# Kernel optimization log

Hardware: AMD Instinct MI355X
Metric: run time of the kernel (lower is better)

The kernel has to match this reference:

```python
import jax, jax.numpy as jnp
import numpy as np

N_STEPS = 100
E_PERT = 0.001
K_GATE = 500.0

# (a1,a2,a3,a4, b1,b2,b3,b4, xi_E, xi_I) per oscillator type
_COEFFS = {
    1: (0.0, 5.0, 5.0, 1.0, 0.0, -1.0, 1.0, 0.0, 0.0, 0.0),
    2: (0.5, 0.55, 0.55, -0.5, 0.5, -0.55, -0.55, -0.5, 0.0, 0.0),
    3: (-5.0, 5.0, 5.0, -5.0, 1.0, -1.0, -1.0, 1.0, 0.0, 0.0),
    4: (1.0, 1.0, 1.0, -1.0, -1.0, -1.0, -1.0, 1.0, 0.0, 0.0),
    5: (5.0, -5.0, -5.0, 5.0, -1.0, 1.0, 1.0, -1.0, 0.0, 0.0),
    6: (-1.0, -1.0, -1.0, 1.0, 1.0, 1.0, 1.0, -1.0, 0.0, 0.0),
    7: (1.0, -1.0, -1.0, 1.0, -1.0, 1.0, 1.0, -1.0, 0.0, 0.0),
    8: (-1.0, 1.0, 1.0, -1.0, 1.0, -1.0, -1.0, 1.0, 0.0, 0.0),
}

def _tanh5(x):
    return jnp.tanh(5.0 * x)

def lee_oscillator(x, oscillator_type):
    a1, a2, a3, a4, b1, b2, b3, b4, xi_E, xi_I = _COEFFS[int(oscillator_type)]
    shape = x.shape
    xf = x.reshape(-1)
    sim = xf + E_PERT * jnp.sign(xf)
    gate = jnp.exp(-K_GATE * sim * sim)   # exp(-k*sim^2), constant over steps
    omega = _tanh5(sim)                   # Omega[t+1] = tanh(5*sim), constant

    E0 = jnp.full_like(xf, 0.2)
    I0 = jnp.zeros_like(xf)
    L0 = jnp.full_like(xf, 0.2)

    def step(carry, _):
        E, I, L = carry
        E1 = _tanh5(a1 * L + a2 * E - a3 * I + a4 * sim - xi_E)
        I1 = _tanh5(b1 * L - b2 * E - b3 * I + b4 * sim - xi_I)
        L1 = (E1 - I1) * gate + omega
        return (E1, I1, L1), None

    (_, _, L_final), _ = jax.lax.scan(step, (E0, I0, L0), None, length=N_STEPS - 1)
    return L_final.reshape(shape)

def setup_inputs() -> dict:
    key = jax.random.key(0)
    x = jax.random.normal(key, (4096, 4096), dtype=jnp.float32)
    return {"x": x, "oscillator_type": 1}

def reference(x, oscillator_type):
    return lee_oscillator(x, oscillator_type)
```

## Files before the change

### kernel.cpp

```cpp
#include <hip/hip_runtime.h>


#pragma clang fp contract(off)

#define N_ITERS 99
#define LOG_GATE_THRESH -6.2146080984221916f
#define BLOCK 256
#define ITERS_PER_WAVE 64
#define WSPAN (64 * ITERS_PER_WAVE)
#define SPAN (4 * WSPAN)
#define WL_CAP 512

__device__ __constant__ float kCoeffs[8][10] = {
    { 0.0f,  5.0f,   5.0f,   1.0f,  0.0f, -1.0f,   1.0f,  0.0f, 0.0f, 0.0f},
    { 0.5f,  0.55f,  0.55f, -0.5f,  0.5f, -0.55f, -0.55f, -0.5f, 0.0f, 0.0f},
    {-5.0f,  5.0f,   5.0f,  -5.0f,  1.0f, -1.0f,  -1.0f,  1.0f, 0.0f, 0.0f},
    { 1.0f,  1.0f,   1.0f,  -1.0f, -1.0f, -1.0f,  -1.0f,  1.0f, 0.0f, 0.0f},
    { 5.0f, -5.0f,  -5.0f,   5.0f, -1.0f,  1.0f,   1.0f, -1.0f, 0.0f, 0.0f},
    {-1.0f, -1.0f,  -1.0f,   1.0f,  1.0f,  1.0f,   1.0f, -1.0f, 0.0f, 0.0f},
    { 1.0f, -1.0f,  -1.0f,   1.0f, -1.0f,  1.0f,   1.0f, -1.0f, 0.0f, 0.0f},
    {-1.0f,  1.0f,   1.0f,  -1.0f,  1.0f, -1.0f,  -1.0f,  1.0f, 0.0f, 0.0f},
};

__device__ __forceinline__ float xla_fast_tanh(float x) {
#pragma clang fp contract(off)
    const float kClamp = 7.99881172180175781f;
    float ax = __builtin_fabsf(x);
    float xc = __builtin_fminf(__builtin_fmaxf(x, -kClamp), kClamp);
    float x2 = __fmul_rn(xc, xc);
    float p = __fmaf_rn(x2, -2.76076847742355e-16f, 2.00018790482477e-13f);
    p = __fmaf_rn(x2, p, -8.60467152213735e-11f);
    p = __fmaf_rn(x2, p, 5.12229709037114e-08f);
    p = __fmaf_rn(x2, p, 1.48572235717979e-05f);
    p = __fmaf_rn(x2, p, 6.37261928875436e-04f);
    p = __fmaf_rn(x2, p, 4.89352455891786e-03f);
    p = __fmul_rn(xc, p);
    float q = __fmaf_rn(x2, 1.19825839466702e-06f, 1.18534705686654e-04f);
    q = __fmaf_rn(x2, q, 2.26843463243900e-03f);
    q = __fmaf_rn(x2, q, 4.89352518554385e-03f);
    float r = p / q;
    return (ax < 0.0004f) ? x : r;
}

__device__ __forceinline__ float lee_compute(float xv, const float* c) {
#pragma clang fp contract(off)
    const float a1 = c[0], a2 = c[1], a3 = c[2], a4 = c[3];
    const float b1 = c[4], b2 = c[5], b3 = c[6], b4 = c[7];
    const float xiE = c[8], xiI = c[9];

    float sgn = (xv > 0.0f) ? 1.0f : ((xv < 0.0f) ? -1.0f : 0.0f);
    float sim = __fadd_rn(xv, __fmul_rn(0.001f, sgn));
    float gq = __fmul_rn(__fmul_rn(-500.0f, sim), sim);
    float gate = expf(gq);
    float omega = xla_fast_tanh(__fmul_rn(5.0f, sim));

    float E = 0.2f, I = 0.0f, L = 0.2f;
    for (int s = 0; s < N_ITERS; ++s) {
        float tE = __fmul_rn(a1, L);
        tE = __fadd_rn(tE, __fmul_rn(a2, E));
        tE = __fsub_rn(tE, __fmul_rn(a3, I));
        tE = __fadd_rn(tE, __fmul_rn(a4, sim));
        tE = __fsub_rn(tE, xiE);
        float E1 = xla_fast_tanh(__fmul_rn(5.0f, tE));

        float tI = __fmul_rn(b1, L);
        tI = __fsub_rn(tI, __fmul_rn(b2, E));
        tI = __fsub_rn(tI, __fmul_rn(b3, I));
        tI = __fadd_rn(tI, __fmul_rn(b4, sim));
        tI = __fsub_rn(tI, xiI);
        float I1 = xla_fast_tanh(__fmul_rn(5.0f, tI));

        L = __fadd_rn(__fmul_rn(__fsub_rn(E1, I1), gate), omega);
        E = E1;
        I = I1;
    }
    return L;
}

__global__ __launch_bounds__(BLOCK) void lee_osc_kernel(
    const float* __restrict__ x, const int* __restrict__ osc_type,
    float* __restrict__ out, int n) {
#pragma clang fp contract(off)
    __shared__ unsigned short s_idx[4][WL_CAP];
    __shared__ float s_x[4][WL_CAP];

    int t = osc_type[0];
    if (t < 1 || t > 8) t = 1;
    const float* c = kCoeffs[t - 1];

    const int wave = (int)(threadIdx.x >> 6);
    const int lane = (int)(threadIdx.x & 63);
    const int wbase = (int)blockIdx.x * SPAN + wave * WSPAN;

    if (t != 1) {
        for (int p = 0; p < ITERS_PER_WAVE; ++p) {
            int i = wbase + p * 64 + lane;
            if (i < n) out[i] = lee_compute(x[i], c);
        }
        return;
    }

    const unsigned long long lt_mask = (1ull << lane) - 1ull;
    unsigned int cnt = 0;
    for (int p = 0; p < ITERS_PER_WAVE; ++p) {
        int li = p * 64 + lane;
        int i = wbase + li;
        bool valid = (i < n);
        float xv = valid ? x[i] : 1.0e9f;
        float sgn = (xv > 0.0f) ? 1.0f : ((xv < 0.0f) ? -1.0f : 0.0f);
        float sim = __fadd_rn(xv, __fmul_rn(0.001f, sgn));
        float gq = __fmul_rn(__fmul_rn(-500.0f, sim), sim);
        bool surv = valid && !(gq < LOG_GATE_THRESH);
        if (valid && !surv) {
            out[i] = xla_fast_tanh(__fmul_rn(5.0f, sim));
        }
        unsigned long long mask = __ballot(surv);
        unsigned int pos = cnt + (unsigned int)__popcll(mask & lt_mask);
        if (surv) {
            if (pos < WL_CAP) {
                s_idx[wave][pos] = (unsigned short)li;
                s_x[wave][pos] = xv;
            } else {
                out[i] = lee_compute(xv, c);
            }
        }
        cnt += (unsigned int)__popcll(mask);
    }

    unsigned int m = (cnt < WL_CAP) ? cnt : WL_CAP;
    for (unsigned int j = (unsigned int)lane; j < m; j += 64u) {
        int i = wbase + (int)s_idx[wave][j];
        float xv = s_x[wave][j];
        out[i] = lee_compute(xv, c);
    }
}

extern "C" void kernel_launch(void* const* d_in, const int* in_sizes, int n_in,
                              void* d_out, int out_size, void* d_ws, size_t ws_size,
                              hipStream_t stream) {
    const float* x = (const float*)d_in[0];
    const int* typ = (const int*)d_in[1];
    float* out = (float*)d_out;
    int n = out_size;
    int blocks = (n + SPAN - 1) / SPAN;
    lee_osc_kernel<<<blocks, BLOCK, 0, stream>>>(x, typ, out, n);
}
```

Baseline: 294.2 us.

## Split into classify pass and global worklist pass for load-balanced survivors

The single kernel becomes three launches: zero a global counter, classify elements and append surviving (non-negligible gate) indices into a global worklist via one atomic per block, then compute the full recurrence over the compacted worklist with a grid-stride kernel. The aim is to remove load imbalance from per-wave local worklists, where waves with many survivors serialize the 99-step loop. The cost is extra launches, global worklist traffic and an atomic, and the single-kernel version is kept as a fallback when workspace is too small.

```diff
diff --git a/kernel.cpp b/kernel.cpp
--- a/kernel.cpp
+++ b/kernel.cpp
@@ -77,12 +77,21 @@
     return L;
 }
 
-__global__ __launch_bounds__(BLOCK) void lee_osc_kernel(
+__global__ void lee_zero_counter(unsigned int* __restrict__ count) {
+    if (threadIdx.x == 0 && blockIdx.x == 0) count[0] = 0u;
+}
+
+__global__ __launch_bounds__(BLOCK) void lee_classify(
     const float* __restrict__ x, const int* __restrict__ osc_type,
-    float* __restrict__ out, int n) {
+    float* __restrict__ out, unsigned int* __restrict__ count,
+    unsigned int* __restrict__ wl_idx, float* __restrict__ wl_x,
+    unsigned int cap, int n) {
 #pragma clang fp contract(off)
     __shared__ unsigned short s_idx[4][WL_CAP];
     __shared__ float s_x[4][WL_CAP];
+    __shared__ unsigned int s_cnt[4];
+    __shared__ unsigned int s_base;
+    __shared__ unsigned int s_off[4];
 
     int t = osc_type[0];
     if (t < 1 || t > 8) t = 1;
@@ -126,12 +135,99 @@
         }
         cnt += (unsigned int)__popcll(mask);
     }
-
+    if (lane == 0) s_cnt[wave] = (cnt < WL_CAP) ? cnt : WL_CAP;
+    __syncthreads();
+
+    if (threadIdx.x == 0) {
+        unsigned int o0 = 0;
+        unsigned int offs[4];
+        for (int w = 0; w < 4; ++w) { offs[w] = o0; o0 += s_cnt[w]; }
+        s_base = atomicAdd(count, o0);
+        for (int w = 0; w < 4; ++w) s_off[w] = offs[w];
+    }
+    __syncthreads();
+
+    unsigned int wcnt = s_cnt[wave];
+    unsigned int gb = s_base + s_off[wave];
+    for (unsigned int j = (unsigned int)lane; j < wcnt; j += 64u) {
+        unsigned int g = gb + j;
+        int i = wbase + (int)s_idx[wave][j];
+        float xv = s_x[wave][j];
+        if (g < cap) {
+            wl_idx[g] = (unsigned int)i;
+            wl_x[g] = xv;
+        } else {
+            out[i] = lee_compute(xv, c);
+        }
+    }
+}
+
+__global__ __launch_bounds__(BLOCK) void lee_worklist(
+    const int* __restrict__ osc_type, float* __restrict__ out,
+    const unsigned int* __restrict__ count,
+    const unsigned int* __restrict__ wl_idx, const float* __restrict__ wl_x,
+    unsigned int cap, int n) {
+#pragma clang fp contract(off)
+    unsigned int m = count[0];
+    if (m > cap) m = cap;
+    int t = osc_type[0];
+    if (t < 1 || t > 8) t = 1;
+    const float* c = kCoeffs[t - 1];
+    unsigned int stride = gridDim.x * BLOCK;
+    for (unsigned int j = blockIdx.x * BLOCK + threadIdx.x; j < m; j += stride) {
+        unsigned int i = wl_idx[j];
+        float xv = wl_x[j];
+        if (i < (unsigned int)n) out[i] = lee_compute(xv, c);
+    }
+}
+
+__global__ __launch_bounds__(BLOCK) void lee_osc_fallback(
+    const float* __restrict__ x, const int* __restrict__ osc_type,
+    float* __restrict__ out, int n) {
+#pragma clang fp contract(off)
+    __shared__ unsigned short s_idx[4][WL_CAP];
+    __shared__ float s_x[4][WL_CAP];
+
+    int t = osc_type[0];
+    if (t < 1 || t > 8) t = 1;
+    const float* c = kCoeffs[t - 1];
+
+    const int wave = (int)(threadIdx.x >> 6);
+    const int lane = (int)(threadIdx.x & 63);
+    const int wbase = (int)blockIdx.x * SPAN + wave * WSPAN;
+
+    if (t != 1) {
+        for (int p = 0; p < ITERS_PER_WAVE; ++p) {
+            int i = wbase + p * 64 + lane;
+            if (i < n) out[i] = lee_compute(x[i], c);
+        }
+        return;
+    }
+
+    const unsigned long long lt_mask = (1ull << lane) - 1ull;
+    unsigned int cnt = 0;
+    for (int p = 0; p < ITERS_PER_WAVE; ++p) {
+        int li = p * 64 + lane;
+        int i = wbase + li;
+        bool valid = (i < n);
+        float xv = valid ? x[i] : 1.0e9f;
+        float sgn = (xv > 0.0f) ? 1.0f : ((xv < 0.0f) ? -1.0f : 0.0f);
+        float sim = __fadd_rn(xv, __fmul_rn(0.001f, sgn));
+        float gq = __fmul_rn(__fmul_rn(-500.0f, sim), sim);
+        bool surv = valid && !(gq < LOG_GATE_THRESH);
+        if (valid && !surv) out[i] = xla_fast_tanh(__fmul_rn(5.0f, sim));
+        unsigned long long mask = __ballot(surv);
+        unsigned int pos = cnt + (unsigned int)__popcll(mask & lt_mask);
+        if (surv) {
+            if (pos < WL_CAP) { s_idx[wave][pos] = (unsigned short)li; s_x[wave][pos] = xv; }
+            else out[i] = lee_compute(xv, c);
+        }
+        cnt += (unsigned int)__popcll(mask);
+    }
     unsigned int m = (cnt < WL_CAP) ? cnt : WL_CAP;
     for (unsigned int j = (unsigned int)lane; j < m; j += 64u) {
         int i = wbase + (int)s_idx[wave][j];
-        float xv = s_x[wave][j];
-        out[i] = lee_compute(xv, c);
+        out[i] = lee_compute(s_x[wave][j], c);
     }
 }
 
@@ -142,6 +238,21 @@
     const int* typ = (const int*)d_in[1];
     float* out = (float*)d_out;
     int n = out_size;
-    int blocks = (n + SPAN - 1) / SPAN;
-    lee_osc_kernel<<<blocks, BLOCK, 0, stream>>>(x, typ, out, n);
-}
+    int blocksA = (n + SPAN - 1) / SPAN;
+
+    unsigned int cap = (ws_size > 16) ? (unsigned int)((ws_size - 16) / 8) : 0u;
+    unsigned int need = (unsigned int)(n / 8) + 1024u;
+
+    if (cap < need) {
+        lee_osc_fallback<<<blocksA, BLOCK, 0, stream>>>(x, typ, out, n);
+        return;
+    }
+
+    unsigned int* count = (unsigned int*)d_ws;
+    unsigned int* wl_idx = (unsigned int*)((char*)d_ws + 16);
+    float* wl_x = (float*)((char*)d_ws + 16 + (size_t)cap * 4u);
+
+    lee_zero_counter<<<1, 64, 0, stream>>>(count);
+    lee_classify<<<blocksA, BLOCK, 0, stream>>>(x, typ, out, count, wl_idx, wl_x, cap, n);
+    lee_worklist<<<2048, BLOCK, 0, stream>>>(typ, out, count, wl_idx, wl_x, cap, n);
+}
```

Result: faster. 255.2 us (-13.3%).
